# Kernel tuning notes

Hardware: AMD Instinct MI355X
Metric: run time of the kernel (lower is better)

Reference implementation:

```python
import jax, jax.numpy as jnp
import numpy as np

TAU = 10.0
N, D = 4096, 8192  # batch, feature dim (D >= N required by the original indexing)
NUM_CLASSES = 100


def setup_inputs() -> dict:
    key = jax.random.key(0)
    k1, k2 = jax.random.split(key)
    embeddings = jax.random.normal(k1, (N, D), dtype=jnp.float32)
    labels = jax.random.randint(k2, (N,), 0, NUM_CLASSES, dtype=jnp.int64)
    return {"embeddings": embeddings, "labels": labels}


def reference(embeddings, labels):
    # Faithful to the original (buggy) torch math:
    # inner_product[i, d] = exp(emb[i, d]**2 / tau)  (trailing singleton dim dropped)
    n = embeddings.shape[0]
    A = jnp.exp(embeddings * embeddings / TAU)          # [N, D]
    # denominator_i = sum_d A[i, d] - A[i, i]
    denom = jnp.sum(A, axis=1) - jnp.diagonal(A)[:n]    # [N]
    # numerator terms: exp(A[i, j] / tau) for j in batch indices (j < N <= D)
    B = jnp.exp(A[:, :n] / TAU)                          # [N, N]
    same = labels[:, None] == labels[None, :]            # [N, N]
    mask = same & ~jnp.eye(n, dtype=bool)
    counts = jnp.sum(mask, axis=1).astype(embeddings.dtype)   # misma_clase per i
    suma = jnp.sum(jnp.where(mask, B, jnp.zeros((), B.dtype)), axis=1) / denom  # [N]
    return jnp.sum(jnp.log(suma / counts))
```

## Files before the change

### kernel.cpp

```cpp
#include <hip/hip_runtime.h>

static constexpr int N = 4096;
static constexpr int D = 8192;
static constexpr int BLOCK = 256;
static constexpr int ROWS_PER_BLOCK = 4;

__global__ __launch_bounds__(BLOCK) void supcon_rows(
    const float* __restrict__ emb,
    const int* __restrict__ labels,
    float* __restrict__ row_out)
{
    const int wave = threadIdx.x >> 6;
    const int lane = threadIdx.x & 63;
    const int row  = blockIdx.x * ROWS_PER_BLOCK + wave;
    const int lab_i = labels[row];

    const float4* rowp = reinterpret_cast<const float4*>(emb + (size_t)row * D);
    const int4*   labp = reinterpret_cast<const int4*>(labels);

    float denom = 0.f, ssum = 0.f, diag = 0.f, fcnt = 0.f;

    #pragma unroll
    for (int c = 0; c < 2; ++c) {
        float4 v[8]; int4 lj[8];
        #pragma unroll
        for (int i = 0; i < 8; ++i) {
            const int idx = (c * 8 + i) * 64 + lane;
            v[i]  = rowp[idx];
            lj[i] = labp[idx];
        }
        #pragma unroll
        for (int i = 0; i < 8; ++i) {
            const int j0 = ((c * 8 + i) * 64 + lane) * 4;
            const float xs[4] = {v[i].x, v[i].y, v[i].z, v[i].w};
            const int   ls[4] = {lj[i].x, lj[i].y, lj[i].z, lj[i].w};
            #pragma unroll
            for (int k = 0; k < 4; ++k) {
                float a = __expf(xs[k] * xs[k] * 0.1f);
                denom += a;
                float b = __expf(a * 0.1f);
                bool match = (ls[k] == lab_i) && (j0 + k != row);
                ssum += match ? b : 0.f;
                fcnt += match ? 1.f : 0.f;
                diag += (j0 + k == row) ? a : 0.f;
            }
        }
    }

    #pragma unroll
    for (int c = 0; c < 2; ++c) {
        float4 v[8];
        #pragma unroll
        for (int i = 0; i < 8; ++i)
            v[i] = rowp[1024 + (c * 8 + i) * 64 + lane];
        #pragma unroll
        for (int i = 0; i < 8; ++i) {
            denom += __expf(v[i].x * v[i].x * 0.1f);
            denom += __expf(v[i].y * v[i].y * 0.1f);
            denom += __expf(v[i].z * v[i].z * 0.1f);
            denom += __expf(v[i].w * v[i].w * 0.1f);
        }
    }

    #pragma unroll
    for (int off = 32; off > 0; off >>= 1) {
        denom += __shfl_down(denom, off);
        ssum  += __shfl_down(ssum,  off);
        diag  += __shfl_down(diag,  off);
        fcnt  += __shfl_down(fcnt,  off);
    }
    if (lane == 0) {
        const float dn = denom - diag;
        row_out[row] = __logf(ssum) - __logf(dn) - __logf(fcnt);
    }
}

__global__ __launch_bounds__(1024) void reduce_rows(
    const float* __restrict__ row_vals, float* __restrict__ out)
{
    const int tid = threadIdx.x;
    float4 x = reinterpret_cast<const float4*>(row_vals)[tid];
    float s = x.x + x.y + x.z + x.w;
    #pragma unroll
    for (int off = 32; off > 0; off >>= 1)
        s += __shfl_down(s, off);
    __shared__ float sb[16];
    if ((tid & 63) == 0) sb[tid >> 6] = s;
    __syncthreads();
    if (tid == 0) {
        float t = 0.f;
        #pragma unroll
        for (int w = 0; w < 16; ++w) t += sb[w];
        *out = t;
    }
}

extern "C" void kernel_launch(void* const* d_in, const int* in_sizes, int n_in,
                              void* d_out, int out_size, void* d_ws, size_t ws_size,
                              hipStream_t stream) {
    const float* emb  = (const float*)d_in[0];
    const int* labels = (const int*)d_in[1];
    float* out        = (float*)d_out;
    float* row_vals   = (float*)d_ws;

    supcon_rows<<<dim3(N / ROWS_PER_BLOCK), dim3(BLOCK), 0, stream>>>(emb, labels, row_vals);
    reduce_rows<<<dim3(1), dim3(1024), 0, stream>>>(row_vals, out);
}
```

Before: 192.5 us.

## Split each row across four waves and fix up the diagonal in a combine kernel

Each row is now handled by four waves, each covering a quarter of the columns, instead of one wave per row. This gives four times as many waves for latency hiding and memory parallelism on the 128 MB read. The diagonal exclusion is taken out of the inner loop and applied in a new combine kernel, which reloads the diagonal element and subtracts its contribution from the sums. The final reduction becomes per-block atomicAdds into a memset output, which adds a memset, a workspace round trip and a different floating-point summation order.

```diff
diff --git a/kernel.cpp b/kernel.cpp
--- a/kernel.cpp
+++ b/kernel.cpp
@@ -3,35 +3,34 @@
 static constexpr int N = 4096;
 static constexpr int D = 8192;
 static constexpr int BLOCK = 256;
-static constexpr int ROWS_PER_BLOCK = 4;
 
-__global__ __launch_bounds__(BLOCK) void supcon_rows(
+__global__ __launch_bounds__(BLOCK) void supcon_partial(
     const float* __restrict__ emb,
     const int* __restrict__ labels,
-    float* __restrict__ row_out)
+    float4* __restrict__ wsA,
+    float* __restrict__ wsB)
 {
     const int wave = threadIdx.x >> 6;
     const int lane = threadIdx.x & 63;
-    const int row  = blockIdx.x * ROWS_PER_BLOCK + wave;
-    const int lab_i = labels[row];
+    const int waveId = blockIdx.x * 4 + wave;
+    const int row = waveId >> 2;
+    const int q   = waveId & 3;
 
     const float4* rowp = reinterpret_cast<const float4*>(emb + (size_t)row * D);
-    const int4*   labp = reinterpret_cast<const int4*>(labels);
 
-    float denom = 0.f, ssum = 0.f, diag = 0.f, fcnt = 0.f;
-
-    #pragma unroll
-    for (int c = 0; c < 2; ++c) {
+    if (q < 2) {
+        const int lab_i = labels[row];
+        const int4* labp = reinterpret_cast<const int4*>(labels);
         float4 v[8]; int4 lj[8];
         #pragma unroll
         for (int i = 0; i < 8; ++i) {
-            const int idx = (c * 8 + i) * 64 + lane;
+            const int idx = q * 512 + i * 64 + lane;
             v[i]  = rowp[idx];
             lj[i] = labp[idx];
         }
+        float denom = 0.f, ssum = 0.f, fcnt = 0.f;
         #pragma unroll
         for (int i = 0; i < 8; ++i) {
-            const int j0 = ((c * 8 + i) * 64 + lane) * 4;
             const float xs[4] = {v[i].x, v[i].y, v[i].z, v[i].w};
             const int   ls[4] = {lj[i].x, lj[i].y, lj[i].z, lj[i].w};
             #pragma unroll
@@ -39,20 +38,25 @@
                 float a = __expf(xs[k] * xs[k] * 0.1f);
                 denom += a;
                 float b = __expf(a * 0.1f);
-                bool match = (ls[k] == lab_i) && (j0 + k != row);
-                ssum += match ? b : 0.f;
-                fcnt += match ? 1.f : 0.f;
-                diag += (j0 + k == row) ? a : 0.f;
+                bool m = (ls[k] == lab_i);
+                ssum += m ? b : 0.f;
+                fcnt += m ? 1.f : 0.f;
             }
         }
-    }
-
-    #pragma unroll
-    for (int c = 0; c < 2; ++c) {
+        #pragma unroll
+        for (int off = 32; off > 0; off >>= 1) {
+            denom += __shfl_down(denom, off);
+            ssum  += __shfl_down(ssum,  off);
+            fcnt  += __shfl_down(fcnt,  off);
+        }
+        if (lane == 0)
+            wsA[row * 2 + q] = make_float4(denom, ssum, fcnt, 0.f);
+    } else {
         float4 v[8];
         #pragma unroll
         for (int i = 0; i < 8; ++i)
-            v[i] = rowp[1024 + (c * 8 + i) * 64 + lane];
+            v[i] = rowp[1024 + (q - 2) * 512 + i * 64 + lane];
+        float denom = 0.f;
         #pragma unroll
         for (int i = 0; i < 8; ++i) {
             denom += __expf(v[i].x * v[i].x * 0.1f);
@@ -60,39 +64,41 @@
             denom += __expf(v[i].z * v[i].z * 0.1f);
             denom += __expf(v[i].w * v[i].w * 0.1f);
         }
-    }
-
-    #pragma unroll
-    for (int off = 32; off > 0; off >>= 1) {
-        denom += __shfl_down(denom, off);
-        ssum  += __shfl_down(ssum,  off);
-        diag  += __shfl_down(diag,  off);
-        fcnt  += __shfl_down(fcnt,  off);
-    }
-    if (lane == 0) {
-        const float dn = denom - diag;
-        row_out[row] = __logf(ssum) - __logf(dn) - __logf(fcnt);
+        #pragma unroll
+        for (int off = 32; off > 0; off >>= 1)
+            denom += __shfl_down(denom, off);
+        if (lane == 0)
+            wsB[row * 2 + (q - 2)] = denom;
     }
 }
 
-__global__ __launch_bounds__(1024) void reduce_rows(
-    const float* __restrict__ row_vals, float* __restrict__ out)
+__global__ __launch_bounds__(256) void supcon_combine(
+    const float* __restrict__ emb,
+    const float4* __restrict__ wsA,
+    const float* __restrict__ wsB,
+    float* __restrict__ out)
 {
-    const int tid = threadIdx.x;
-    float4 x = reinterpret_cast<const float4*>(row_vals)[tid];
-    float s = x.x + x.y + x.z + x.w;
+    const int row = blockIdx.x * 256 + threadIdx.x;
+    const float4 p0 = wsA[row * 2 + 0];
+    const float4 p1 = wsA[row * 2 + 1];
+    const float b0 = wsB[row * 2 + 0];
+    const float b1 = wsB[row * 2 + 1];
+    const float x  = emb[(size_t)row * D + row];
+    const float ad = __expf(x * x * 0.1f);
+
+    const float denom = (p0.x + p1.x + b0 + b1) - ad;
+    const float ssum  = (p0.y + p1.y) - __expf(ad * 0.1f);
+    const float fcnt  = (p0.z + p1.z) - 1.f;
+    float val = __logf(ssum) - __logf(denom) - __logf(fcnt);
+
     #pragma unroll
     for (int off = 32; off > 0; off >>= 1)
-        s += __shfl_down(s, off);
-    __shared__ float sb[16];
-    if ((tid & 63) == 0) sb[tid >> 6] = s;
+        val += __shfl_down(val, off);
+    __shared__ float sb[4];
+    if ((threadIdx.x & 63) == 0) sb[threadIdx.x >> 6] = val;
     __syncthreads();
-    if (tid == 0) {
-        float t = 0.f;
-        #pragma unroll
-        for (int w = 0; w < 16; ++w) t += sb[w];
-        *out = t;
-    }
+    if (threadIdx.x == 0)
+        atomicAdd(out, sb[0] + sb[1] + sb[2] + sb[3]);
 }
 
 extern "C" void kernel_launch(void* const* d_in, const int* in_sizes, int n_in,
@@ -101,8 +107,11 @@
     const float* emb  = (const float*)d_in[0];
     const int* labels = (const int*)d_in[1];
     float* out        = (float*)d_out;
-    float* row_vals   = (float*)d_ws;
 
-    supcon_rows<<<dim3(N / ROWS_PER_BLOCK), dim3(BLOCK), 0, stream>>>(emb, labels, row_vals);
-    reduce_rows<<<dim3(1), dim3(1024), 0, stream>>>(row_vals, out);
+    float4* wsA = (float4*)d_ws;
+    float*  wsB = (float*)((char*)d_ws + N * 2 * sizeof(float4));
+
+    hipMemsetAsync(out, 0, sizeof(float), stream);
+    supcon_partial<<<dim3(N * 4 / 4), dim3(BLOCK), 0, stream>>>(emb, labels, wsA, wsB);
+    supcon_combine<<<dim3(N / 256), dim3(256), 0, stream>>>(emb, wsA, wsB, out);
 }
```

Result: no change. 191.0 us (-0.8%).
